# Performance work log

Measured on AMD Instinct MI355X. Metric: run time of the kernel, lower is better.

The kernel has to match this reference:

```python
import jax, jax.numpy as jnp
import numpy as np

N_NODES = 50000
N_EDGES = 400000
DIM = 64
HEADS = 4
BN_EPS = 1e-5


def glorot(key, shape, fan_in, fan_out):
    std = np.sqrt(6.0 / (fan_in + fan_out))
    return jax.random.uniform(key, shape, jnp.float32, -std, std)


def setup_inputs() -> dict:
    key = jax.random.key(0)
    ks = jax.random.split(key, 6)
    x = jax.random.normal(ks[0], (N_NODES, DIM), jnp.float32)
    edge_attr = jax.random.normal(ks[1], (N_EDGES, DIM), jnp.float32)
    edge_index = jax.random.randint(ks[2], (2, N_EDGES), 0, N_NODES, jnp.int64)
    W = glorot(ks[3], (2 * DIM, HEADS * DIM), 2 * DIM, HEADS * DIM)
    att = glorot(ks[4], (1, HEADS, 2 * DIM), 2 * DIM, 1)
    bias = jnp.zeros((DIM,), jnp.float32)
    bn_gamma = jnp.ones((HEADS,), jnp.float32)
    bn_beta = jnp.zeros((HEADS,), jnp.float32)
    return {"x": x, "edge_attr": edge_attr, "W": W, "att": att,
            "bias": bias, "bn_gamma": bn_gamma, "bn_beta": bn_beta,
            "edge_index": edge_index}


def segment_softmax(a, seg, num_segments):
    # numerically stable softmax over variable-size neighborhoods (per segment)
    m = jax.ops.segment_max(a, seg, num_segments=num_segments)
    e = jnp.exp(a - m[seg])
    s = jax.ops.segment_sum(e, seg, num_segments=num_segments)
    return e / (s[seg] + 1e-16)


def reference(x, edge_attr, W, att, bias, bn_gamma, bn_beta, edge_index):
    act = jax.nn.softplus
    i, j = edge_index[0], edge_index[1]  # flow='target_to_source': i indexes x_i and aggregation
    x_i = x[i]                           # [E, D]
    x_j = x[j]                           # [E, D]
    out_i = act(jnp.concatenate([x_i, edge_attr], -1) @ W).reshape(-1, HEADS, DIM)
    out_j = act(jnp.concatenate([x_j, edge_attr], -1) @ W).reshape(-1, HEADS, DIM)
    # attention logits: [E, H]
    alpha = act((jnp.concatenate([out_i, out_j], -1) * att).sum(-1))
    # BatchNorm1d over heads with batch statistics (biased variance)
    mu = alpha.mean(0)
    var = alpha.var(0)
    alpha = (alpha - mu) * jax.lax.rsqrt(var + BN_EPS) * bn_gamma + bn_beta
    alpha = act(alpha)
    alpha = segment_softmax(alpha, i, N_NODES)     # softmax per target node
    msg = out_j * alpha[:, :, None]                # [E, H, D]
    aggr = jax.ops.segment_sum(msg, i, num_segments=N_NODES)  # [N, H, D]
    out = aggr.mean(1) + bias                      # mean over heads, then bias
    return out
```

## Files before the change

### kernel.cpp

```cpp
#include <hip/hip_runtime.h>
#include <hip/hip_bf16.h>

#define NN 50000
#define NE 400000

static const size_t OFF_ALPHA  = 0;
static const size_t OFF_SEGSUM = 6400000;
static const size_t OFF_BN     = 7200000;
static const size_t OFF_AGGR   = 7200256;
static const size_t OFF_IDX32  = 20000256;
static const size_t OFF_WT     = 23200256;
static const size_t OFF_XB     = 23265792;
static const size_t OFF_EAB    = 29665792;
static const size_t Z_SZ       = OFF_IDX32 - OFF_SEGSUM;

typedef __attribute__((ext_vector_type(8))) __bf16 bf16x8;
typedef __attribute__((ext_vector_type(4))) float  f32x4;
typedef __attribute__((ext_vector_type(4))) int    i32x4;
typedef __attribute__((ext_vector_type(2))) unsigned u32x2;

#define L2E 1.44269504f
#define LN2 0.69314718f

__device__ __forceinline__ float fexp2(float x) {
  float r; asm("v_exp_f32 %0, %1" : "=v"(r) : "v"(x)); return r;
}
__device__ __forceinline__ float flog2(float x) {
  float r; asm("v_log_f32 %0, %1" : "=v"(r) : "v"(x)); return r;
}
__device__ __forceinline__ float softplusf(float x) {
  return fmaxf(x, 0.0f) + LN2 * flog2(1.0f + fexp2(-L2E * fabsf(x)));
}
__device__ __forceinline__ float expsp(float y) {
  return fexp2(L2E * fmaxf(y, 0.0f)) * (1.0f + fexp2(-L2E * fabsf(y)));
}
__device__ __forceinline__ unsigned bfbits(float f) {
  return (unsigned)__builtin_bit_cast(unsigned short, __float2bfloat16(f));
}
__device__ __forceinline__ unsigned pkbf(float a, float b) {
  return bfbits(a) | (bfbits(b) << 16);
}
__device__ __forceinline__ bf16x8 ld8(const unsigned short* p) {
  return __builtin_bit_cast(bf16x8, *reinterpret_cast<const i32x4*>(p));
}
#define MFMA __builtin_amdgcn_mfma_f32_16x16x32_bf16

__global__ __launch_bounds__(256)
void k_idx_detect(const unsigned* __restrict__ src, unsigned* __restrict__ flag)
{
  int t = blockIdx.x * 256 + threadIdx.x;
  unsigned v = (t < NE) ? src[2 * t + 1] : 0u;
  if (__any(v != 0)) { if ((threadIdx.x & 63) == 0) atomicOr(flag, 1u); }
}
__global__ __launch_bounds__(256)
void k_idx_cvt(const unsigned* __restrict__ src, const unsigned* __restrict__ flag,
               int* __restrict__ dst)
{
  int e = blockIdx.x * 256 + threadIdx.x;
  unsigned f = *flag;
  dst[e] = (int)(f ? src[e] : src[2 * e]);
}

__global__ __launch_bounds__(256)
void k_wprep(const float* __restrict__ W, __hip_bfloat16* __restrict__ wt)
{
  int t = blockIdx.x * 256 + threadIdx.x;
  int k = t >> 8, c = t & 255;
  wt[c * 128 + k] = __float2bfloat16(W[t]);
}

__global__ __launch_bounds__(256)
void k_cvt_bf16(const float* __restrict__ src, unsigned* __restrict__ dst)
{
  int t = blockIdx.x * 256 + threadIdx.x;
  f32x4 v = *reinterpret_cast<const f32x4*>(src + (size_t)t * 4);
  u32x2 p = { pkbf(v[0], v[1]), pkbf(v[2], v[3]) };
  *reinterpret_cast<u32x2*>(dst + (size_t)t * 2) = p;
}

__global__ __launch_bounds__(256, 3)
void k_edge_alpha(const __hip_bfloat16* __restrict__ xb,
                  const __hip_bfloat16* __restrict__ eab,
                  const __hip_bfloat16* __restrict__ wt,
                  const float* __restrict__ att, const int* __restrict__ idx,
                  float* __restrict__ alpha, float* __restrict__ bnst)
{
  __shared__ float attl[512];
  __shared__ float red[32];
  for (int t = threadIdx.x; t < 512; t += 256) attl[t] = att[t];
  __syncthreads();
  const int wave = threadIdx.x >> 6, lane = threadIdx.x & 63;
  const int m = lane & 15, rg = lane >> 4;
  const unsigned short* xbu = reinterpret_cast<const unsigned short*>(xb);
  const unsigned short* eau = reinterpret_cast<const unsigned short*>(eab);
  const unsigned short* wtu = reinterpret_cast<const unsigned short*>(wt);
  const int e0 = blockIdx.x * 128 + wave * 32;

  const int iA = idx[e0 + m],      jA = idx[NE + e0 + m];
  const int iB = idx[e0 + 16 + m], jB = idx[NE + e0 + 16 + m];
  bf16x8 xiA0 = ld8(xbu + (size_t)iA * 64 + rg * 8);
  bf16x8 xiA1 = ld8(xbu + (size_t)iA * 64 + 32 + rg * 8);
  bf16x8 xjA0 = ld8(xbu + (size_t)jA * 64 + rg * 8);
  bf16x8 xjA1 = ld8(xbu + (size_t)jA * 64 + 32 + rg * 8);
  bf16x8 eA0  = ld8(eau + (size_t)(e0 + m) * 64 + rg * 8);
  bf16x8 eA1  = ld8(eau + (size_t)(e0 + m) * 64 + 32 + rg * 8);
  bf16x8 xiB0 = ld8(xbu + (size_t)iB * 64 + rg * 8);
  bf16x8 xiB1 = ld8(xbu + (size_t)iB * 64 + 32 + rg * 8);
  bf16x8 xjB0 = ld8(xbu + (size_t)jB * 64 + rg * 8);
  bf16x8 xjB1 = ld8(xbu + (size_t)jB * 64 + 32 + rg * 8);
  bf16x8 eB0  = ld8(eau + (size_t)(e0 + 16 + m) * 64 + rg * 8);
  bf16x8 eB1  = ld8(eau + (size_t)(e0 + 16 + m) * 64 + 32 + rg * 8);

  f32x4 pA0 = {0.f,0.f,0.f,0.f}, pA1 = pA0, pA2 = pA0, pA3 = pA0;
  f32x4 pB0 = pA0, pB1 = pA0, pB2 = pA0, pB3 = pA0;

#pragma unroll
  for (int t = 0; t < 16; ++t) {
    const unsigned short* wp = wtu + (t * 16 + m) * 128 + rg * 8;
    bf16x8 bx0 = ld8(wp);
    bf16x8 bx1 = ld8(wp + 32);
    bf16x8 be0 = ld8(wp + 64);
    bf16x8 be1 = ld8(wp + 96);
    f32x4 ciA = {0.f,0.f,0.f,0.f};
    ciA = MFMA(xiA0, bx0, ciA, 0, 0, 0);
    ciA = MFMA(xiA1, bx1, ciA, 0, 0, 0);
    ciA = MFMA(eA0,  be0, ciA, 0, 0, 0);
    ciA = MFMA(eA1,  be1, ciA, 0, 0, 0);
    f32x4 cjA = {0.f,0.f,0.f,0.f};
    cjA = MFMA(xjA0, bx0, cjA, 0, 0, 0);
    cjA = MFMA(xjA1, bx1, cjA, 0, 0, 0);
    cjA = MFMA(eA0,  be0, cjA, 0, 0, 0);
    cjA = MFMA(eA1,  be1, cjA, 0, 0, 0);
    f32x4 ciB = {0.f,0.f,0.f,0.f};
    ciB = MFMA(xiB0, bx0, ciB, 0, 0, 0);
    ciB = MFMA(xiB1, bx1, ciB, 0, 0, 0);
    ciB = MFMA(eB0,  be0, ciB, 0, 0, 0);
    ciB = MFMA(eB1,  be1, ciB, 0, 0, 0);
    f32x4 cjB = {0.f,0.f,0.f,0.f};
    cjB = MFMA(xjB0, bx0, cjB, 0, 0, 0);
    cjB = MFMA(xjB1, bx1, cjB, 0, 0, 0);
    cjB = MFMA(eB0,  be0, cjB, 0, 0, 0);
    cjB = MFMA(eB1,  be1, cjB, 0, 0, 0);
    const int h = t >> 2;
    const float ai = attl[h * 128 + (t & 3) * 16 + m];
    const float aj = attl[h * 128 + 64 + (t & 3) * 16 + m];
    pA0[h] = fmaf(softplusf(ciA[0]), ai, fmaf(softplusf(cjA[0]), aj, pA0[h]));
    pA1[h] = fmaf(softplusf(ciA[1]), ai, fmaf(softplusf(cjA[1]), aj, pA1[h]));
    pA2[h] = fmaf(softplusf(ciA[2]), ai, fmaf(softplusf(cjA[2]), aj, pA2[h]));
    pA3[h] = fmaf(softplusf(ciA[3]), ai, fmaf(softplusf(cjA[3]), aj, pA3[h]));
    pB0[h] = fmaf(softplusf(ciB[0]), ai, fmaf(softplusf(cjB[0]), aj, pB0[h]));
    pB1[h] = fmaf(softplusf(ciB[1]), ai, fmaf(softplusf(cjB[1]), aj, pB1[h]));
    pB2[h] = fmaf(softplusf(ciB[2]), ai, fmaf(softplusf(cjB[2]), aj, pB2[h]));
    pB3[h] = fmaf(softplusf(ciB[3]), ai, fmaf(softplusf(cjB[3]), aj, pB3[h]));
  }

  float bs = 0.f, ss = 0.f;
#pragma unroll
  for (int h = 0; h < 4; ++h) {
    pA0[h] += __shfl_xor(pA0[h], 1); pA0[h] += __shfl_xor(pA0[h], 2);
    pA0[h] += __shfl_xor(pA0[h], 4); pA0[h] += __shfl_xor(pA0[h], 8);
    pA1[h] += __shfl_xor(pA1[h], 1); pA1[h] += __shfl_xor(pA1[h], 2);
    pA1[h] += __shfl_xor(pA1[h], 4); pA1[h] += __shfl_xor(pA1[h], 8);
    pA2[h] += __shfl_xor(pA2[h], 1); pA2[h] += __shfl_xor(pA2[h], 2);
    pA2[h] += __shfl_xor(pA2[h], 4); pA2[h] += __shfl_xor(pA2[h], 8);
    pA3[h] += __shfl_xor(pA3[h], 1); pA3[h] += __shfl_xor(pA3[h], 2);
    pA3[h] += __shfl_xor(pA3[h], 4); pA3[h] += __shfl_xor(pA3[h], 8);
    pB0[h] += __shfl_xor(pB0[h], 1); pB0[h] += __shfl_xor(pB0[h], 2);
    pB0[h] += __shfl_xor(pB0[h], 4); pB0[h] += __shfl_xor(pB0[h], 8);
    pB1[h] += __shfl_xor(pB1[h], 1); pB1[h] += __shfl_xor(pB1[h], 2);
    pB1[h] += __shfl_xor(pB1[h], 4); pB1[h] += __shfl_xor(pB1[h], 8);
    pB2[h] += __shfl_xor(pB2[h], 1); pB2[h] += __shfl_xor(pB2[h], 2);
    pB2[h] += __shfl_xor(pB2[h], 4); pB2[h] += __shfl_xor(pB2[h], 8);
    pB3[h] += __shfl_xor(pB3[h], 1); pB3[h] += __shfl_xor(pB3[h], 2);
    pB3[h] += __shfl_xor(pB3[h], 4); pB3[h] += __shfl_xor(pB3[h], 8);
  }
  if (m < 4) {
    float vA0 = (m == 0) ? pA0[0] : (m == 1) ? pA0[1] : (m == 2) ? pA0[2] : pA0[3];
    float vA1 = (m == 0) ? pA1[0] : (m == 1) ? pA1[1] : (m == 2) ? pA1[2] : pA1[3];
    float vA2 = (m == 0) ? pA2[0] : (m == 1) ? pA2[1] : (m == 2) ? pA2[2] : pA2[3];
    float vA3 = (m == 0) ? pA3[0] : (m == 1) ? pA3[1] : (m == 2) ? pA3[2] : pA3[3];
    float vB0 = (m == 0) ? pB0[0] : (m == 1) ? pB0[1] : (m == 2) ? pB0[2] : pB0[3];
    float vB1 = (m == 0) ? pB1[0] : (m == 1) ? pB1[1] : (m == 2) ? pB1[2] : pB1[3];
    float vB2 = (m == 0) ? pB2[0] : (m == 1) ? pB2[1] : (m == 2) ? pB2[2] : pB2[3];
    float vB3 = (m == 0) ? pB3[0] : (m == 1) ? pB3[1] : (m == 2) ? pB3[2] : pB3[3];
    vA0 = softplusf(vA0); vA1 = softplusf(vA1); vA2 = softplusf(vA2); vA3 = softplusf(vA3);
    vB0 = softplusf(vB0); vB1 = softplusf(vB1); vB2 = softplusf(vB2); vB3 = softplusf(vB3);
    alpha[(size_t)(e0 + rg * 4 + 0) * 4 + m] = vA0;
    alpha[(size_t)(e0 + rg * 4 + 1) * 4 + m] = vA1;
    alpha[(size_t)(e0 + rg * 4 + 2) * 4 + m] = vA2;
    alpha[(size_t)(e0 + rg * 4 + 3) * 4 + m] = vA3;
    alpha[(size_t)(e0 + 16 + rg * 4 + 0) * 4 + m] = vB0;
    alpha[(size_t)(e0 + 16 + rg * 4 + 1) * 4 + m] = vB1;
    alpha[(size_t)(e0 + 16 + rg * 4 + 2) * 4 + m] = vB2;
    alpha[(size_t)(e0 + 16 + rg * 4 + 3) * 4 + m] = vB3;
    bs = vA0 + vA1 + vA2 + vA3 + vB0 + vB1 + vB2 + vB3;
    ss = vA0*vA0 + vA1*vA1 + vA2*vA2 + vA3*vA3 + vB0*vB0 + vB1*vB1 + vB2*vB2 + vB3*vB3;
  }
  bs += __shfl_xor(bs, 16); bs += __shfl_xor(bs, 32);
  ss += __shfl_xor(ss, 16); ss += __shfl_xor(ss, 32);
  if (lane < 4) { red[wave * 8 + lane] = bs; red[wave * 8 + 4 + lane] = ss; }
  __syncthreads();
  if (threadIdx.x < 8) {
    float s = red[threadIdx.x] + red[8 + threadIdx.x] + red[16 + threadIdx.x] + red[24 + threadIdx.x];
    atomicAdd(&bnst[threadIdx.x], s);
  }
}

__global__ void k_bn_fin(float* __restrict__ bnst, const float* __restrict__ gamma)
{
  int q = threadIdx.x;
  if (q < 4) {
    float mu = bnst[q] * (1.0f / NE);
    float var = bnst[4 + q] * (1.0f / NE) - mu * mu;
    bnst[8 + q] = mu;
    bnst[12 + q] = rsqrtf(var + 1e-5f) * gamma[q];
  }
}

__global__ __launch_bounds__(256)
void k_bn_expsum(float* __restrict__ alpha, const int* __restrict__ idx,
                 const float* __restrict__ bnst, const float* __restrict__ beta,
                 float* __restrict__ segsum)
{
  int e = blockIdx.x * 256 + threadIdx.x;
  if (e >= NE) return;
  float4 a = *reinterpret_cast<const float4*>(&alpha[(size_t)e * 4]);
  int n = idx[e];
  a.x = expsp((a.x - bnst[8])  * bnst[12] + beta[0]);
  a.y = expsp((a.y - bnst[9])  * bnst[13] + beta[1]);
  a.z = expsp((a.z - bnst[10]) * bnst[14] + beta[2]);
  a.w = expsp((a.w - bnst[11]) * bnst[15] + beta[3]);
  *reinterpret_cast<float4*>(&alpha[(size_t)e * 4]) = a;
  atomicAdd(&segsum[n * 4 + 0], a.x);
  atomicAdd(&segsum[n * 4 + 1], a.y);
  atomicAdd(&segsum[n * 4 + 2], a.z);
  atomicAdd(&segsum[n * 4 + 3], a.w);
}

__global__ __launch_bounds__(256, 3)
void k_edge_aggr(const __hip_bfloat16* __restrict__ xb,
                 const __hip_bfloat16* __restrict__ eab,
                 const __hip_bfloat16* __restrict__ wt,
                 const int* __restrict__ idx, const float* __restrict__ alpha,
                 const float* __restrict__ segsum, float* __restrict__ aggr)
{
  const int wave = threadIdx.x >> 6, lane = threadIdx.x & 63;
  const int m = lane & 15, rg = lane >> 4;
  const unsigned short* xbu = reinterpret_cast<const unsigned short*>(xb);
  const unsigned short* eau = reinterpret_cast<const unsigned short*>(eab);
  const unsigned short* wtu = reinterpret_cast<const unsigned short*>(wt);
  const int e0 = blockIdx.x * 128 + wave * 32;

  const int jA = idx[NE + e0 + m], jB = idx[NE + e0 + 16 + m];
  bf16x8 xjA0 = ld8(xbu + (size_t)jA * 64 + rg * 8);
  bf16x8 xjA1 = ld8(xbu + (size_t)jA * 64 + 32 + rg * 8);
  bf16x8 eA0  = ld8(eau + (size_t)(e0 + m) * 64 + rg * 8);
  bf16x8 eA1  = ld8(eau + (size_t)(e0 + m) * 64 + 32 + rg * 8);
  bf16x8 xjB0 = ld8(xbu + (size_t)jB * 64 + rg * 8);
  bf16x8 xjB1 = ld8(xbu + (size_t)jB * 64 + 32 + rg * 8);
  bf16x8 eB0  = ld8(eau + (size_t)(e0 + 16 + m) * 64 + rg * 8);
  bf16x8 eB1  = ld8(eau + (size_t)(e0 + 16 + m) * 64 + 32 + rg * 8);

  const int iA0 = idx[e0 + rg * 4 + 0];
  const int iA1 = idx[e0 + rg * 4 + 1];
  const int iA2 = idx[e0 + rg * 4 + 2];
  const int iA3 = idx[e0 + rg * 4 + 3];
  const int iB0 = idx[e0 + 16 + rg * 4 + 0];
  const int iB1 = idx[e0 + 16 + rg * 4 + 1];
  const int iB2 = idx[e0 + 16 + rg * 4 + 2];
  const int iB3 = idx[e0 + 16 + rg * 4 + 3];

  f32x4 wA0, wA1, wA2, wA3, wB0, wB1, wB2, wB3;
  {
    f32x4 ev0 = *reinterpret_cast<const f32x4*>(alpha + (size_t)(e0 + rg * 4 + 0) * 4);
    f32x4 ev1 = *reinterpret_cast<const f32x4*>(alpha + (size_t)(e0 + rg * 4 + 1) * 4);
    f32x4 ev2 = *reinterpret_cast<const f32x4*>(alpha + (size_t)(e0 + rg * 4 + 2) * 4);
    f32x4 ev3 = *reinterpret_cast<const f32x4*>(alpha + (size_t)(e0 + rg * 4 + 3) * 4);
    f32x4 fv0 = *reinterpret_cast<const f32x4*>(alpha + (size_t)(e0 + 16 + rg * 4 + 0) * 4);
    f32x4 fv1 = *reinterpret_cast<const f32x4*>(alpha + (size_t)(e0 + 16 + rg * 4 + 1) * 4);
    f32x4 fv2 = *reinterpret_cast<const f32x4*>(alpha + (size_t)(e0 + 16 + rg * 4 + 2) * 4);
    f32x4 fv3 = *reinterpret_cast<const f32x4*>(alpha + (size_t)(e0 + 16 + rg * 4 + 3) * 4);
    f32x4 sA0 = *reinterpret_cast<const f32x4*>(segsum + (size_t)iA0 * 4);
    f32x4 sA1 = *reinterpret_cast<const f32x4*>(segsum + (size_t)iA1 * 4);
    f32x4 sA2 = *reinterpret_cast<const f32x4*>(segsum + (size_t)iA2 * 4);
    f32x4 sA3 = *reinterpret_cast<const f32x4*>(segsum + (size_t)iA3 * 4);
    f32x4 sB0 = *reinterpret_cast<const f32x4*>(segsum + (size_t)iB0 * 4);
    f32x4 sB1 = *reinterpret_cast<const f32x4*>(segsum + (size_t)iB1 * 4);
    f32x4 sB2 = *reinterpret_cast<const f32x4*>(segsum + (size_t)iB2 * 4);
    f32x4 sB3 = *reinterpret_cast<const f32x4*>(segsum + (size_t)iB3 * 4);
#pragma unroll
    for (int h = 0; h < 4; ++h) {
      wA0[h] = 0.25f * ev0[h] / (sA0[h] + 1e-16f);
      wA1[h] = 0.25f * ev1[h] / (sA1[h] + 1e-16f);
      wA2[h] = 0.25f * ev2[h] / (sA2[h] + 1e-16f);
      wA3[h] = 0.25f * ev3[h] / (sA3[h] + 1e-16f);
      wB0[h] = 0.25f * fv0[h] / (sB0[h] + 1e-16f);
      wB1[h] = 0.25f * fv1[h] / (sB1[h] + 1e-16f);
      wB2[h] = 0.25f * fv2[h] / (sB2[h] + 1e-16f);
      wB3[h] = 0.25f * fv3[h] / (sB3[h] + 1e-16f);
    }
  }

  f32x4 cA0 = {0.f,0.f,0.f,0.f}, cA1 = cA0, cA2 = cA0, cA3 = cA0;
  f32x4 cB0 = cA0, cB1 = cA0, cB2 = cA0, cB3 = cA0;

#pragma unroll
  for (int t = 0; t < 16; ++t) {
    const unsigned short* wp = wtu + (t * 16 + m) * 128 + rg * 8;
    bf16x8 bx0 = ld8(wp);
    bf16x8 bx1 = ld8(wp + 32);
    bf16x8 be0 = ld8(wp + 64);
    bf16x8 be1 = ld8(wp + 96);
    f32x4 cjA = {0.f,0.f,0.f,0.f};
    cjA = MFMA(xjA0, bx0, cjA, 0, 0, 0);
    cjA = MFMA(xjA1, bx1, cjA, 0, 0, 0);
    cjA = MFMA(eA0,  be0, cjA, 0, 0, 0);
    cjA = MFMA(eA1,  be1, cjA, 0, 0, 0);
    f32x4 cjB = {0.f,0.f,0.f,0.f};
    cjB = MFMA(xjB0, bx0, cjB, 0, 0, 0);
    cjB = MFMA(xjB1, bx1, cjB, 0, 0, 0);
    cjB = MFMA(eB0,  be0, cjB, 0, 0, 0);
    cjB = MFMA(eB1,  be1, cjB, 0, 0, 0);
    const int h = t >> 2, tq = t & 3;
    cA0[tq] = fmaf(softplusf(cjA[0]), wA0[h], cA0[tq]);
    cA1[tq] = fmaf(softplusf(cjA[1]), wA1[h], cA1[tq]);
    cA2[tq] = fmaf(softplusf(cjA[2]), wA2[h], cA2[tq]);
    cA3[tq] = fmaf(softplusf(cjA[3]), wA3[h], cA3[tq]);
    cB0[tq] = fmaf(softplusf(cjB[0]), wB0[h], cB0[tq]);
    cB1[tq] = fmaf(softplusf(cjB[1]), wB1[h], cB1[tq]);
    cB2[tq] = fmaf(softplusf(cjB[2]), wB2[h], cB2[tq]);
    cB3[tq] = fmaf(softplusf(cjB[3]), wB3[h], cB3[tq]);
  }

#pragma unroll
  for (int tq = 0; tq < 4; ++tq) {
    atomicAdd(&aggr[(size_t)iA0 * 64 + tq * 16 + m], cA0[tq]);
    atomicAdd(&aggr[(size_t)iA1 * 64 + tq * 16 + m], cA1[tq]);
    atomicAdd(&aggr[(size_t)iA2 * 64 + tq * 16 + m], cA2[tq]);
    atomicAdd(&aggr[(size_t)iA3 * 64 + tq * 16 + m], cA3[tq]);
    atomicAdd(&aggr[(size_t)iB0 * 64 + tq * 16 + m], cB0[tq]);
    atomicAdd(&aggr[(size_t)iB1 * 64 + tq * 16 + m], cB1[tq]);
    atomicAdd(&aggr[(size_t)iB2 * 64 + tq * 16 + m], cB2[tq]);
    atomicAdd(&aggr[(size_t)iB3 * 64 + tq * 16 + m], cB3[tq]);
  }
}

__global__ __launch_bounds__(256)
void k_final(const float* __restrict__ aggr, const float* __restrict__ bias,
             float* __restrict__ out)
{
  int t = blockIdx.x * 256 + threadIdx.x;
  out[t] = aggr[t] + bias[t & 63];
}

extern "C" void kernel_launch(void* const* d_in, const int* in_sizes, int n_in,
                              void* d_out, int out_size, void* d_ws, size_t ws_size,
                              hipStream_t stream)
{
  const float* x    = (const float*)d_in[0];
  const float* ea   = (const float*)d_in[1];
  const float* W    = (const float*)d_in[2];
  const float* att  = (const float*)d_in[3];
  const float* bias = (const float*)d_in[4];
  const float* gam  = (const float*)d_in[5];
  const float* bet  = (const float*)d_in[6];
  const unsigned* idx_raw = (const unsigned*)d_in[7];
  float* out = (float*)d_out;

  char* ws = (char*)d_ws;
  float*    alpha  = (float*)(ws + OFF_ALPHA);
  float*    segsum = (float*)(ws + OFF_SEGSUM);
  float*    bnst   = (float*)(ws + OFF_BN);
  unsigned* flag   = (unsigned*)(ws + OFF_BN + 64);
  float*    aggr   = (float*)(ws + OFF_AGGR);
  int*      idx    = (int*)(ws + OFF_IDX32);
  __hip_bfloat16* wt  = (__hip_bfloat16*)(ws + OFF_WT);
  __hip_bfloat16* xb  = (__hip_bfloat16*)(ws + OFF_XB);
  __hip_bfloat16* eab = (__hip_bfloat16*)(ws + OFF_EAB);

  hipMemsetAsync(ws + OFF_SEGSUM, 0, Z_SZ, stream);
  k_wprep<<<128, 256, 0, stream>>>(W, wt);
  k_idx_detect<<<(NE + 255) / 256, 256, 0, stream>>>(idx_raw, flag);
  k_idx_cvt<<<(2 * NE) / 256, 256, 0, stream>>>(idx_raw, flag, idx);
  k_cvt_bf16<<<(NN * 64 / 4) / 256, 256, 0, stream>>>(x, (unsigned*)xb);
  k_cvt_bf16<<<(NE * 64 / 4) / 256, 256, 0, stream>>>(ea, (unsigned*)eab);

  k_edge_alpha<<<NE / 128, 256, 0, stream>>>(xb, eab, wt, att, idx, alpha, bnst);
  k_bn_fin<<<1, 64, 0, stream>>>(bnst, gam);
  k_bn_expsum<<<(NE + 255) / 256, 256, 0, stream>>>(alpha, idx, bnst, bet, segsum);
  k_edge_aggr<<<NE / 128, 256, 0, stream>>>(xb, eab, wt, idx, alpha, segsum, aggr);
  k_final<<<(NN * 64) / 256, 256, 0, stream>>>(aggr, bias, out);
}
```

Baseline: 478.4 us.

## Stage transposed weights in LDS and use 512-thread blocks for edge kernels

Both MFMA edge kernels now copy the bf16 weight matrix into padded shared memory once per block instead of each wave reading it from global memory. Blocks are doubled to 512 threads covering 256 edges, with an out-of-bounds guard for the partial last block. The aim is to cut repeated global/L1 weight traffic. In exchange it adds a per-block staging cost and uses roughly 70KB of LDS per block, which limits occupancy.

```diff
diff --git a/kernel.cpp b/kernel.cpp
--- a/kernel.cpp
+++ b/kernel.cpp
@@ -3,6 +3,7 @@
 
 #define NN 50000
 #define NE 400000
+#define WTP 136
 
 static const size_t OFF_ALPHA  = 0;
 static const size_t OFF_SEGSUM = 6400000;
@@ -78,23 +79,38 @@
   *reinterpret_cast<u32x2*>(dst + (size_t)t * 2) = p;
 }
 
-__global__ __launch_bounds__(256, 3)
+__device__ __forceinline__ void stage_wt(unsigned short* wtl,
+                                         const unsigned short* wtu, int tid)
+{
+  for (int it = tid; it < 4096; it += 512) {
+    int c = it >> 4, k8 = (it & 15) << 3;
+    *reinterpret_cast<i32x4*>(&wtl[c * WTP + k8]) =
+        *reinterpret_cast<const i32x4*>(wtu + c * 128 + k8);
+  }
+}
+
+__global__ __launch_bounds__(512, 4)
 void k_edge_alpha(const __hip_bfloat16* __restrict__ xb,
                   const __hip_bfloat16* __restrict__ eab,
                   const __hip_bfloat16* __restrict__ wt,
                   const float* __restrict__ att, const int* __restrict__ idx,
                   float* __restrict__ alpha, float* __restrict__ bnst)
 {
+  __shared__ __align__(16) unsigned short wtl[256 * WTP];
   __shared__ float attl[512];
-  __shared__ float red[32];
-  for (int t = threadIdx.x; t < 512; t += 256) attl[t] = att[t];
+  __shared__ float red[64];
+  const unsigned short* wtu = reinterpret_cast<const unsigned short*>(wt);
+  stage_wt(wtl, wtu, threadIdx.x);
+  if (threadIdx.x < 512) attl[threadIdx.x] = att[threadIdx.x];
   __syncthreads();
+
   const int wave = threadIdx.x >> 6, lane = threadIdx.x & 63;
   const int m = lane & 15, rg = lane >> 4;
   const unsigned short* xbu = reinterpret_cast<const unsigned short*>(xb);
   const unsigned short* eau = reinterpret_cast<const unsigned short*>(eab);
-  const unsigned short* wtu = reinterpret_cast<const unsigned short*>(wt);
-  const int e0 = blockIdx.x * 128 + wave * 32;
+  const int e0r = blockIdx.x * 256 + wave * 32;
+  const bool oob = (e0r >= NE);
+  const int e0 = oob ? 0 : e0r;
 
   const int iA = idx[e0 + m],      jA = idx[NE + e0 + m];
   const int iB = idx[e0 + 16 + m], jB = idx[NE + e0 + 16 + m];
@@ -116,7 +132,7 @@
 
 #pragma unroll
   for (int t = 0; t < 16; ++t) {
-    const unsigned short* wp = wtu + (t * 16 + m) * 128 + rg * 8;
+    const unsigned short* wp = wtl + (t * 16 + m) * WTP + rg * 8;
     bf16x8 bx0 = ld8(wp);
     bf16x8 bx1 = ld8(wp + 32);
     bf16x8 be0 = ld8(wp + 64);
@@ -185,23 +201,27 @@
     float vB3 = (m == 0) ? pB3[0] : (m == 1) ? pB3[1] : (m == 2) ? pB3[2] : pB3[3];
     vA0 = softplusf(vA0); vA1 = softplusf(vA1); vA2 = softplusf(vA2); vA3 = softplusf(vA3);
     vB0 = softplusf(vB0); vB1 = softplusf(vB1); vB2 = softplusf(vB2); vB3 = softplusf(vB3);
-    alpha[(size_t)(e0 + rg * 4 + 0) * 4 + m] = vA0;
-    alpha[(size_t)(e0 + rg * 4 + 1) * 4 + m] = vA1;
-    alpha[(size_t)(e0 + rg * 4 + 2) * 4 + m] = vA2;
-    alpha[(size_t)(e0 + rg * 4 + 3) * 4 + m] = vA3;
-    alpha[(size_t)(e0 + 16 + rg * 4 + 0) * 4 + m] = vB0;
-    alpha[(size_t)(e0 + 16 + rg * 4 + 1) * 4 + m] = vB1;
-    alpha[(size_t)(e0 + 16 + rg * 4 + 2) * 4 + m] = vB2;
-    alpha[(size_t)(e0 + 16 + rg * 4 + 3) * 4 + m] = vB3;
-    bs = vA0 + vA1 + vA2 + vA3 + vB0 + vB1 + vB2 + vB3;
-    ss = vA0*vA0 + vA1*vA1 + vA2*vA2 + vA3*vA3 + vB0*vB0 + vB1*vB1 + vB2*vB2 + vB3*vB3;
+    if (!oob) {
+      alpha[(size_t)(e0 + rg * 4 + 0) * 4 + m] = vA0;
+      alpha[(size_t)(e0 + rg * 4 + 1) * 4 + m] = vA1;
+      alpha[(size_t)(e0 + rg * 4 + 2) * 4 + m] = vA2;
+      alpha[(size_t)(e0 + rg * 4 + 3) * 4 + m] = vA3;
+      alpha[(size_t)(e0 + 16 + rg * 4 + 0) * 4 + m] = vB0;
+      alpha[(size_t)(e0 + 16 + rg * 4 + 1) * 4 + m] = vB1;
+      alpha[(size_t)(e0 + 16 + rg * 4 + 2) * 4 + m] = vB2;
+      alpha[(size_t)(e0 + 16 + rg * 4 + 3) * 4 + m] = vB3;
+      bs = vA0 + vA1 + vA2 + vA3 + vB0 + vB1 + vB2 + vB3;
+      ss = vA0*vA0 + vA1*vA1 + vA2*vA2 + vA3*vA3 + vB0*vB0 + vB1*vB1 + vB2*vB2 + vB3*vB3;
+    }
   }
   bs += __shfl_xor(bs, 16); bs += __shfl_xor(bs, 32);
   ss += __shfl_xor(ss, 16); ss += __shfl_xor(ss, 32);
   if (lane < 4) { red[wave * 8 + lane] = bs; red[wave * 8 + 4 + lane] = ss; }
   __syncthreads();
   if (threadIdx.x < 8) {
-    float s = red[threadIdx.x] + red[8 + threadIdx.x] + red[16 + threadIdx.x] + red[24 + threadIdx.x];
+    float s = 0.f;
+#pragma unroll
+    for (int w2 = 0; w2 < 8; ++w2) s += red[w2 * 8 + threadIdx.x];
     atomicAdd(&bnst[threadIdx.x], s);
   }
 }
@@ -237,19 +257,25 @@
   atomicAdd(&segsum[n * 4 + 3], a.w);
 }
 
-__global__ __launch_bounds__(256, 3)
+__global__ __launch_bounds__(512, 4)
 void k_edge_aggr(const __hip_bfloat16* __restrict__ xb,
                  const __hip_bfloat16* __restrict__ eab,
                  const __hip_bfloat16* __restrict__ wt,
                  const int* __restrict__ idx, const float* __restrict__ alpha,
                  const float* __restrict__ segsum, float* __restrict__ aggr)
 {
+  __shared__ __align__(16) unsigned short wtl[256 * WTP];
+  const unsigned short* wtu = reinterpret_cast<const unsigned short*>(wt);
+  stage_wt(wtl, wtu, threadIdx.x);
+  __syncthreads();
+
   const int wave = threadIdx.x >> 6, lane = threadIdx.x & 63;
   const int m = lane & 15, rg = lane >> 4;
   const unsigned short* xbu = reinterpret_cast<const unsigned short*>(xb);
   const unsigned short* eau = reinterpret_cast<const unsigned short*>(eab);
-  const unsigned short* wtu = reinterpret_cast<const unsigned short*>(wt);
-  const int e0 = blockIdx.x * 128 + wave * 32;
+  const int e0r = blockIdx.x * 256 + wave * 32;
+  const bool oob = (e0r >= NE);
+  const int e0 = oob ? 0 : e0r;
 
   const int jA = idx[NE + e0 + m], jB = idx[NE + e0 + 16 + m];
   bf16x8 xjA0 = ld8(xbu + (size_t)jA * 64 + rg * 8);
@@ -306,7 +332,7 @@
 
 #pragma unroll
   for (int t = 0; t < 16; ++t) {
-    const unsigned short* wp = wtu + (t * 16 + m) * 128 + rg * 8;
+    const unsigned short* wp = wtl + (t * 16 + m) * WTP + rg * 8;
     bf16x8 bx0 = ld8(wp);
     bf16x8 bx1 = ld8(wp + 32);
     bf16x8 be0 = ld8(wp + 64);
@@ -332,16 +358,18 @@
     cB3[tq] = fmaf(softplusf(cjB[3]), wB3[h], cB3[tq]);
   }
 
-#pragma unroll
-  for (int tq = 0; tq < 4; ++tq) {
-    atomicAdd(&aggr[(size_t)iA0 * 64 + tq * 16 + m], cA0[tq]);
-    atomicAdd(&aggr[(size_t)iA1 * 64 + tq * 16 + m], cA1[tq]);
-    atomicAdd(&aggr[(size_t)iA2 * 64 + tq * 16 + m], cA2[tq]);
-    atomicAdd(&aggr[(size_t)iA3 * 64 + tq * 16 + m], cA3[tq]);
-    atomicAdd(&aggr[(size_t)iB0 * 64 + tq * 16 + m], cB0[tq]);
-    atomicAdd(&aggr[(size_t)iB1 * 64 + tq * 16 + m], cB1[tq]);
-    atomicAdd(&aggr[(size_t)iB2 * 64 + tq * 16 + m], cB2[tq]);
-    atomicAdd(&aggr[(size_t)iB3 * 64 + tq * 16 + m], cB3[tq]);
+  if (!oob) {
+#pragma unroll
+    for (int tq = 0; tq < 4; ++tq) {
+      atomicAdd(&aggr[(size_t)iA0 * 64 + tq * 16 + m], cA0[tq]);
+      atomicAdd(&aggr[(size_t)iA1 * 64 + tq * 16 + m], cA1[tq]);
+      atomicAdd(&aggr[(size_t)iA2 * 64 + tq * 16 + m], cA2[tq]);
+      atomicAdd(&aggr[(size_t)iA3 * 64 + tq * 16 + m], cA3[tq]);
+      atomicAdd(&aggr[(size_t)iB0 * 64 + tq * 16 + m], cB0[tq]);
+      atomicAdd(&aggr[(size_t)iB1 * 64 + tq * 16 + m], cB1[tq]);
+      atomicAdd(&aggr[(size_t)iB2 * 64 + tq * 16 + m], cB2[tq]);
+      atomicAdd(&aggr[(size_t)iB3 * 64 + tq * 16 + m], cB3[tq]);
+    }
   }
 }
 
@@ -385,9 +413,10 @@
   k_cvt_bf16<<<(NN * 64 / 4) / 256, 256, 0, stream>>>(x, (unsigned*)xb);
   k_cvt_bf16<<<(NE * 64 / 4) / 256, 256, 0, stream>>>(ea, (unsigned*)eab);
 
-  k_edge_alpha<<<NE / 128, 256, 0, stream>>>(xb, eab, wt, att, idx, alpha, bnst);
+  const int NB = (NE + 255) / 256;
+  k_edge_alpha<<<NB, 512, 0, stream>>>(xb, eab, wt, att, idx, alpha, bnst);
   k_bn_fin<<<1, 64, 0, stream>>>(bnst, gam);
   k_bn_expsum<<<(NE + 255) / 256, 256, 0, stream>>>(alpha, idx, bnst, bet, segsum);
-  k_edge_aggr<<<NE / 128, 256, 0, stream>>>(xb, eab, wt, idx, alpha, segsum, aggr);
+  k_edge_aggr<<<NB, 512, 0, stream>>>(xb, eab, wt, idx, alpha, segsum, aggr);
   k_final<<<(NN * 64) / 256, 256, 0, stream>>>(aggr, bias, out);
 }
```

New measurement: 851.9 us. +78.1%, slower.
